# Performance work log

Measured on AMD Instinct MI355X. Metric: run time of the kernel, lower is better.

Reference implementation:

```python
import jax, jax.numpy as jnp
import numpy as np

B_, L_, O_, N_, S_, U_, DEL, HID, K = 16, 128, 128, 256, 64, 32, 64, 512, 4
D_OUT = DEL + N_ * U_ + N_ * S_  # 24640


def setup_inputs() -> dict:
    key = jax.random.key(0)
    ks = jax.random.split(key, 12)
    return {
        "x": jax.random.normal(ks[0], (B_, O_ + L_, S_), jnp.float32),
        "u": jax.random.normal(ks[1], (B_, 2 * L_, U_), jnp.float32),
        "A": jax.random.normal(ks[2], (N_, 1), jnp.float32) / 20.0,
        "W0": jax.random.normal(ks[3], (HID, S_), jnp.float32) * 0.05,
        "b0": jnp.zeros((HID,), jnp.float32),
        "W1": jax.random.normal(ks[4], (N_, HID), jnp.float32) * 0.05,
        "b1": jnp.zeros((N_,), jnp.float32),
        "conv_w": jax.random.normal(ks[5], (N_ + U_, 1, K), jnp.float32) * 0.3,
        "conv_b": jnp.zeros((N_ + U_,), jnp.float32),
        "Wg": jax.random.normal(ks[6], (D_OUT, N_ + U_), jnp.float32) * 0.05,
        "bg": jnp.zeros((D_OUT,), jnp.float32),
        "Wdt": jax.random.normal(ks[7], (N_, DEL), jnp.float32) * 0.05,
        "bdt": jnp.zeros((N_,), jnp.float32),
    }


def reference(x, u, A, W0, b0, W1, b1, conv_w, conv_b, Wg, bg, Wdt, bdt):
    def proj_x(v):  # Linear -> relu -> Linear (project_x)
        return jax.nn.relu(v @ W0.T + b0) @ W1.T + b1

    u = u[:, :, :U_]
    z0 = proj_x(x[:, O_ - 1, :])                       # (B, N)

    # ---- generate_matrices ----
    x_all = proj_x(x[:, :O_ - 1, :])                   # (B, O-1, N)
    u_all = u[:, :O_ - 1, :]                           # (B, O-1, U)
    old = jax.nn.silu(jnp.concatenate([x_all, u_all], axis=2))  # (B, O-1, N+U)
    old = jnp.transpose(old, (0, 2, 1))                # (B, N+U, O-1)
    old = jax.lax.conv_general_dilated(
        old, conv_w, window_strides=(1,), padding=[(K - 1, K - 1)],
        dimension_numbers=("NCH", "OIH", "NCH"), feature_group_count=N_ + U_,
    ) + conv_b[None, :, None]
    old = old[:, :, -L_:]                              # last L timesteps
    old = jax.nn.silu(jnp.transpose(old, (0, 2, 1)))   # (B, L, N+U)
    gen = old @ Wg.T + bg                              # (B, L, delta + N*U + N*S)
    delta, Bm, Cm = jnp.split(gen, [DEL, DEL + N_ * U_], axis=-1)
    delta = jax.nn.softplus(delta @ Wdt.T + bdt)       # (B, L, N)
    Bm = Bm.reshape(B_, L_, N_, U_)
    Cm = Cm.reshape(B_, L_, N_, S_)

    # ---- discretion_matrices ----
    a = A[:, 0]
    a = -jnp.where(a > 0, a, jnp.expm1(a))             # -celu(A), alpha=1
    dA = jnp.exp(delta * a)                            # (B, L, N)
    dB = ((dA - 1.0) * (1.0 / a))[..., None] * Bm      # (B, L, N, U)

    # ---- selective_scan ----
    u0 = u[:, O_ - 1:O_ - 1 + L_, :]                   # (B, L, U)
    xt = x[:, O_:O_ + L_, :]                           # (B, L, S) targets

    def step(z, inp):
        dAi, dBi, ui, Ci, xti = inp
        z = z * dAi + jnp.einsum("bnu,bu->bn", dBi, ui)
        y = jnp.einsum("bns,bn->bs", Ci, z)
        return z, (y, jnp.mean((y - xti) ** 2))

    xs = (
        jnp.swapaxes(dA, 0, 1), jnp.swapaxes(dB, 0, 1),
        jnp.swapaxes(u0, 0, 1), jnp.swapaxes(Cm, 0, 1), jnp.swapaxes(xt, 0, 1),
    )
    _, (ys, ls) = jax.lax.scan(step, z0, xs)
    loss = jnp.sum(ls) / L_
    return loss, jax.lax.stop_gradient(ys)             # ys: (L, B, S), detached as in torch
```

## Files before the change

### kernel.cpp

```cpp
#include <hip/hip_runtime.h>
#include <math.h>

#define B_   16
#define L_   128
#define O_   128
#define N_   256
#define S_   64
#define U_   32
#define DEL_ 64
#define HID_ 512
#define CH_  288
#define M_   2048
#define KD_  288
#define CM_BASE (DEL_ + N_*U_)
#define NSLICE 32

typedef __bf16 bf16_t;
typedef bf16_t bf16x8 __attribute__((ext_vector_type(8)));
typedef float  f32x4  __attribute__((ext_vector_type(4)));

#define AS1(p) ((const __attribute__((address_space(1))) void*)(unsigned long long)(const void*)(p))
#define AS3(p) ((__attribute__((address_space(3))) void*)(unsigned int)(unsigned long long)(const void*)(p))

__device__ __forceinline__ float silu_f(float x){ return x / (1.f + expf(-x)); }
__device__ __forceinline__ float softplus_f(float x){
  return fmaxf(x, 0.f) + log1pf(expf(-fabsf(x)));
}

__device__ __forceinline__ void cvt8(const float* src, bf16_t* dst){
  float4 a = ((const float4*)src)[0];
  float4 b = ((const float4*)src)[1];
  bf16x8 o;
  o[0]=(bf16_t)a.x; o[1]=(bf16_t)a.y; o[2]=(bf16_t)a.z; o[3]=(bf16_t)a.w;
  o[4]=(bf16_t)b.x; o[5]=(bf16_t)b.y; o[6]=(bf16_t)b.z; o[7]=(bf16_t)b.w;
  *(bf16x8*)dst = o;
}

#define CVT_BLOCKS 3465
#define W0_BLOCKS  16
#define W1_BLOCKS  64
#define XB_BLOCKS  64
__global__ void k_prep(const float* __restrict__ Wg, bf16_t* __restrict__ Wgbf,
                       const float* __restrict__ W0, bf16_t* __restrict__ W0bf,
                       const float* __restrict__ W1, bf16_t* __restrict__ W1bf,
                       const float* __restrict__ x,  bf16_t* __restrict__ xbf,
                       float* __restrict__ lossa){
  if (blockIdx.x == 0 && threadIdx.x < 2) lossa[threadIdx.x] = 0.f;
  if (blockIdx.x < CVT_BLOCKS) {
    int i = blockIdx.x*256 + threadIdx.x;
    if (i >= 887040) return;
    cvt8(Wg + (size_t)i*8, Wgbf + (size_t)i*8);
  } else if (blockIdx.x < CVT_BLOCKS + W0_BLOCKS) {
    int i = (blockIdx.x - CVT_BLOCKS)*256 + threadIdx.x;
    if (i >= 4096) return;
    cvt8(W0 + (size_t)i*8, W0bf + (size_t)i*8);
  } else if (blockIdx.x < CVT_BLOCKS + W0_BLOCKS + W1_BLOCKS) {
    int i = (blockIdx.x - CVT_BLOCKS - W0_BLOCKS)*256 + threadIdx.x;
    if (i >= 16384) return;
    cvt8(W1 + (size_t)i*8, W1bf + (size_t)i*8);
  } else {
    int i = (blockIdx.x - CVT_BLOCKS - W0_BLOCKS - W1_BLOCKS)*256 + threadIdx.x;
    if (i >= 16384) return;
    int m = i >> 3, c0 = (i & 7)*8;
    int b = m >> 7, t = m & 127;
    cvt8(x + (size_t)(((b<<8)+t)<<6) + c0, xbf + (size_t)m*64 + c0);
  }
}

#define STAGE64K(GBASE, ROW0G, STRIDE, KK, LDSP)                                     \
  { const bf16_t* gp_ = (GBASE) + (size_t)((ROW0G) + wave*16 + lm)*(STRIDE) + (KK) + lq*8; \
    __builtin_amdgcn_global_load_lds(AS1(gp_), AS3((LDSP) + wave*512), 16, 0, 0); }

#define STAGE128(GBASE, ROW0G, STRIDE, TT, BUF)                                      \
  { _Pragma("unroll")                                                                \
    for (int kb_ = 0; kb_ < 4; kb_++) {                                              \
      const bf16_t* gp_ = (GBASE) + (size_t)((ROW0G) + wave*16 + lm)*(STRIDE)        \
                          + (TT)*128 + kb_*32 + lq*8;                                \
      __builtin_amdgcn_global_load_lds(AS1(gp_), AS3((BUF) + kb_*2048 + wave*512), 16, 0, 0);\
    } }

#define STAGE32(GBASE, ROW0G, KK, LDSP)                                              \
  { _Pragma("unroll")                                                                \
    for (int l_ = 0; l_ < 2; l_++) {                                                 \
      int g_ = wave*2 + l_;                                                          \
      const bf16_t* gp_ = (GBASE) + (size_t)((ROW0G) + g_*16 + lm)*KD_ + (KK) + lq*8;\
      __builtin_amdgcn_global_load_lds(AS1(gp_), AS3((LDSP) + g_*512), 16, 0, 0);    \
    } }

#define STAGE_FR96(GBASE, ROW0G, KK, LDSP)                                           \
  { _Pragma("unroll")                                                                \
    for (int c_ = 0; c_ < 3; c_++) {                                                 \
      _Pragma("unroll")                                                              \
      for (int q_ = 0; q_ < 2; q_++) {                                               \
        int g_ = wave*2 + q_;                                                        \
        const bf16_t* gp_ = (GBASE) + (size_t)((ROW0G) + g_*16 + lm)*KD_ + (KK) + c_*32 + lq*8;\
        __builtin_amdgcn_global_load_lds(AS1(gp_), AS3((LDSP) + c_*4096 + g_*512), 16, 0, 0);\
      } } }

__global__ __launch_bounds__(256) void k_mlp1m(
    const bf16_t* __restrict__ xbf, const bf16_t* __restrict__ W0bf,
    const float* __restrict__ b0, bf16_t* __restrict__ Hbf){
  __shared__ __align__(16) bf16_t As[2][2048];
  __shared__ __align__(16) bf16_t Bs[2][2048];
  int tid = threadIdx.x;
  int wave = tid >> 6, lane = tid & 63;
  int wm = wave & 1, wn = wave >> 1;
  int nt = blockIdx.x, mt = blockIdx.y;
  int m0 = mt*64, n0 = nt*64;
  int lm = lane & 15, lq = lane >> 4;

  f32x4 acc[2][2];
  #pragma unroll
  for (int i=0;i<2;i++)
    #pragma unroll
    for (int j=0;j<2;j++){ acc[i][j][0]=0.f;acc[i][j][1]=0.f;acc[i][j][2]=0.f;acc[i][j][3]=0.f; }

  STAGE64K(xbf,  m0, 64, 0, As[0]);
  STAGE64K(W0bf, n0, 64, 0, Bs[0]);
  __syncthreads();
  #pragma unroll
  for (int t = 0; t < 2; ++t) {
    int cur = t & 1;
    if (t < 1) {
      STAGE64K(xbf,  m0, 64, 32, As[1]);
      STAGE64K(W0bf, n0, 64, 32, Bs[1]);
    }
    bf16x8 af[2], bff[2];
    #pragma unroll
    for (int i=0;i<2;i++) af[i]  = *(const bf16x8*)&As[cur][(wm*2 + i)*512 + lane*8];
    #pragma unroll
    for (int j=0;j<2;j++) bff[j] = *(const bf16x8*)&Bs[cur][(wn*2 + j)*512 + lane*8];
    #pragma unroll
    for (int i=0;i<2;i++)
      #pragma unroll
      for (int j=0;j<2;j++)
        acc[i][j] = __builtin_amdgcn_mfma_f32_16x16x32_bf16(af[i], bff[j], acc[i][j], 0,0,0);
    __syncthreads();
  }
  #pragma unroll
  for (int i=0;i<2;i++)
    #pragma unroll
    for (int j=0;j<2;j++){
      int col = n0 + wn*32 + j*16 + lm;
      float bb = b0[col];
      #pragma unroll
      for (int r=0;r<4;r++){
        int row = m0 + wm*32 + i*16 + lq*4 + r;
        Hbf[(size_t)row*HID_ + col] = (bf16_t)fmaxf(acc[i][j][r] + bb, 0.f);
      }
    }
}

__global__ __launch_bounds__(256) void k_mlp2m(
    const bf16_t* __restrict__ Hbf, const bf16_t* __restrict__ W1bf,
    const float* __restrict__ b1, float* __restrict__ P){
  __shared__ __align__(16) bf16_t As[2][8192];
  __shared__ __align__(16) bf16_t Bs[2][8192];
  int tid = threadIdx.x;
  int wave = tid >> 6, lane = tid & 63;
  int wm = wave & 1, wn = wave >> 1;
  int nt = blockIdx.x, mt = blockIdx.y;
  int m0 = mt*64, n0 = nt*64;
  int lm = lane & 15, lq = lane >> 4;

  f32x4 acc[2][2];
  #pragma unroll
  for (int i=0;i<2;i++)
    #pragma unroll
    for (int j=0;j<2;j++){ acc[i][j][0]=0.f;acc[i][j][1]=0.f;acc[i][j][2]=0.f;acc[i][j][3]=0.f; }

  STAGE128(Hbf,  m0, HID_, 0, As[0]);
  STAGE128(W1bf, n0, HID_, 0, Bs[0]);
  __syncthreads();
  #pragma unroll
  for (int t = 0; t < 4; ++t) {
    int cur = t & 1;
    if (t < 3) {
      STAGE128(Hbf,  m0, HID_, t+1, As[cur^1]);
      STAGE128(W1bf, n0, HID_, t+1, Bs[cur^1]);
    }
    #pragma unroll
    for (int kb = 0; kb < 4; kb++) {
      bf16x8 af[2], bff[2];
      #pragma unroll
      for (int i=0;i<2;i++) af[i]  = *(const bf16x8*)&As[cur][kb*2048 + (wm*2 + i)*512 + lane*8];
      #pragma unroll
      for (int j=0;j<2;j++) bff[j] = *(const bf16x8*)&Bs[cur][kb*2048 + (wn*2 + j)*512 + lane*8];
      #pragma unroll
      for (int i=0;i<2;i++)
        #pragma unroll
        for (int j=0;j<2;j++)
          acc[i][j] = __builtin_amdgcn_mfma_f32_16x16x32_bf16(af[i], bff[j], acc[i][j], 0,0,0);
    }
    __syncthreads();
  }
  #pragma unroll
  for (int i=0;i<2;i++)
    #pragma unroll
    for (int j=0;j<2;j++){
      int col = n0 + wn*32 + j*16 + lm;
      float bb = b1[col];
      #pragma unroll
      for (int r=0;r<4;r++){
        int row = m0 + wm*32 + i*16 + lq*4 + r;
        P[(size_t)row*N_ + col] = acc[i][j][r] + bb;
      }
    }
}

__global__ __launch_bounds__(256) void k_convdelta(
    const float* __restrict__ P, const float* __restrict__ u,
    const float* __restrict__ cw, const float* __restrict__ cb,
    const float* __restrict__ Wg, const float* __restrict__ bg,
    const float* __restrict__ Wdt, const float* __restrict__ bdt,
    const float* __restrict__ Ap, bf16_t* __restrict__ oldbf,
    float* __restrict__ dA, float* __restrict__ coef){
  __shared__ __align__(16) float olds[4*KD_];
  __shared__ float dr[4][64];
  int tid = threadIdx.x;
  int m0 = blockIdx.x * 4;
  int b = m0 >> 7, l0 = m0 & 127;
  for (int e = tid; e < 4*CH_; e += 256) {
    int r = e / CH_, c = e - r*CH_;
    int l = l0 + r;
    float acc = cb[c];
    #pragma unroll
    for (int k = 0; k < 4; k++) {
      int t = l + k - 1;
      if (t >= 0 && t <= O_-2) {
        float s = (c < N_) ? P[((b<<7)+t)*N_ + c] : u[((b<<8)+t)*U_ + (c-N_)];
        acc += silu_f(s) * cw[c*4 + k];
      }
    }
    float v = silu_f(acc);
    olds[e] = v;
    oldbf[(size_t)(m0+r)*CH_ + c] = (bf16_t)v;
  }
  __syncthreads();
  {
    int d = tid & 63;
    int r = tid >> 6;
    const float* wrow = Wg + (size_t)d*KD_;
    const float* orow = olds + r*KD_;
    float s = 0.f;
    for (int k = 0; k < KD_; k++) s += orow[k] * wrow[k];
    dr[r][d] = s + bg[d];
  }
  __syncthreads();
  int n = tid;
  float wrow[64];
  #pragma unroll
  for (int d = 0; d < 64; d++) wrow[d] = Wdt[n*64 + d];
  float a0 = Ap[n];
  float a = -(a0 > 0.f ? a0 : expm1f(a0));
  float inva = 1.f / a;
  float bd = bdt[n];
  #pragma unroll
  for (int r = 0; r < 4; r++) {
    float s = bd;
    #pragma unroll
    for (int d = 0; d < 64; d++) s += dr[r][d] * wrow[d];
    float dd = softplus_f(s);
    float e  = expf(dd * a);
    size_t m = m0 + r;
    dA[m*N_ + n]   = e;
    coef[m*N_ + n] = (e - 1.f) * inva;
  }
}

__global__ __launch_bounds__(256, 2) void k_bmfma(
    const bf16_t* __restrict__ oldbf, const bf16_t* __restrict__ Wgbf,
    const float* __restrict__ bg, const float* __restrict__ u,
    const float* __restrict__ coef, const float* __restrict__ dAg,
    const float* __restrict__ Pg, float* __restrict__ zall){
  __shared__ union {
    struct { __align__(16) bf16_t A[2][4096]; __align__(16) bf16_t B[2][4096]; } st;
    struct { float wl[128][4]; float dal[128][4]; } sc;
  } sm;
  int tid = threadIdx.x;
  int wave = tid >> 6, lane = tid & 63;
  int wm = wave & 1, wn = wave >> 1;
  int mt = blockIdx.y, nt = blockIdx.x;
  int m0 = mt*128, ncol0 = nt*128;
  int lm = lane & 15, lq = lane >> 4;

  f32x4 acc[4][4];
  #pragma unroll
  for (int i=0;i<4;i++)
    #pragma unroll
    for (int j=0;j<4;j++){ acc[i][j][0]=0.f;acc[i][j][1]=0.f;acc[i][j][2]=0.f;acc[i][j][3]=0.f; }

  STAGE32(oldbf, m0, 0, sm.st.A[0]);
  STAGE32(Wgbf, DEL_ + ncol0, 0, sm.st.B[0]);
  __syncthreads();
  for (int t = 0; t < 9; ++t) {
    int cur = t & 1;
    if (t < 8) {
      int kk = (t+1)*32;
      STAGE32(oldbf, m0, kk, sm.st.A[cur^1]);
      STAGE32(Wgbf, DEL_ + ncol0, kk, sm.st.B[cur^1]);
    }
    bf16x8 af[4], bff[4];
    #pragma unroll
    for (int i=0;i<4;i++) af[i]  = *(const bf16x8*)&sm.st.A[cur][(wm*4 + i)*512 + lane*8];
    #pragma unroll
    for (int j=0;j<4;j++) bff[j] = *(const bf16x8*)&sm.st.B[cur][(wn*4 + j)*512 + lane*8];
    __builtin_amdgcn_s_setprio(1);
    #pragma unroll
    for (int i=0;i<4;i++)
      #pragma unroll
      for (int j=0;j<4;j++)
        acc[i][j] = __builtin_amdgcn_mfma_f32_16x16x32_bf16(af[i], bff[j], acc[i][j], 0,0,0);
    __builtin_amdgcn_s_setprio(0);
    __syncthreads();
  }

  for (int e = tid; e < 512; e += 256)
    sm.sc.dal[e>>2][e&3] = dAg[(size_t)(m0 + (e>>2))*N_ + nt*4 + (e&3)];

  float bgv[4];
  #pragma unroll
  for (int j=0;j<4;j++) bgv[j] = bg[DEL_ + ncol0 + wn*64 + j*16 + lm];
  float p[2][4][4];
  #pragma unroll
  for (int a=0;a<2;a++)
    #pragma unroll
    for (int i=0;i<4;i++)
      #pragma unroll
      for (int r=0;r<4;r++) p[a][i][r]=0.f;
  #pragma unroll
  for (int i=0;i<4;i++){
    #pragma unroll
    for (int r=0;r<4;r++){
      int m = m0 + wm*64 + i*16 + lq*4 + r;
      int b = m >> 7, l = m & 127;
      const float* urow = u + ((size_t)(b<<8) + 127 + l)*U_;
      #pragma unroll
      for (int j=0;j<4;j++){
        float uu = urow[(j&1)*16 + lm];
        p[j>>1][i][r] += (acc[i][j][r] + bgv[j]) * uu;
      }
    }
  }
  #pragma unroll
  for (int mk = 1; mk < 16; mk <<= 1){
    #pragma unroll
    for (int a=0;a<2;a++)
      #pragma unroll
      for (int i=0;i<4;i++)
        #pragma unroll
        for (int r=0;r<4;r++) p[a][i][r] += __shfl_xor(p[a][i][r], mk);
  }
  if (lm == 0){
    #pragma unroll
    for (int nl=0;nl<2;nl++){
      int n = ((ncol0 + wn*64 + nl*32) >> 5);
      int nc = wn*2 + nl;
      #pragma unroll
      for (int i=0;i<4;i++)
        #pragma unroll
        for (int r=0;r<4;r++){
          int l = wm*64 + i*16 + lq*4 + r;
          sm.sc.wl[l][nc] = coef[(size_t)(m0+l)*N_ + n] * p[nl][i][r];
        }
    }
  }
  __syncthreads();

  {
    int nc = wave;
    int n = nt*4 + nc;
    float z0 = Pg[(size_t)(m0 + 127)*N_ + n];
    int l0 = lane*2;
    float a0 = sm.sc.dal[l0][nc],   w0 = sm.sc.wl[l0][nc];
    float a1 = sm.sc.dal[l0+1][nc], w1 = sm.sc.wl[l0+1][nc];
    float A = a0*a1, Bv = w0*a1 + w1;
    #pragma unroll
    for (int d = 1; d < 64; d <<= 1){
      float Ap = __shfl_up(A, d);
      float Bp = __shfl_up(Bv, d);
      if (lane >= d){ Bv = Bp*A + Bv; A = Ap*A; }
    }
    float Ae = __shfl_up(A, 1);
    float Be = __shfl_up(Bv, 1);
    if (lane == 0){ Ae = 1.f; Be = 0.f; }
    float zp = z0*Ae + Be;
    float za = zp*a0 + w0;
    float zb = za*a1 + w1;
    zall[(size_t)(m0 + l0)*N_ + n]     = za;
    zall[(size_t)(m0 + l0 + 1)*N_ + n] = zb;
  }
}

__global__ __launch_bounds__(256, 2) void k_cmfma(
    const bf16_t* __restrict__ oldbf, const bf16_t* __restrict__ Wgbf,
    const float* __restrict__ bg, const float* __restrict__ zall,
    float* __restrict__ ypart){
  __shared__ union {
    struct { __align__(16) bf16_t A[3*4096];
             __align__(16) bf16_t Bb[3*4096];
             float zl[128][8]; } st;
    float ylds[128][64];
  } sm;
  int tid = threadIdx.x;
  int wave = tid >> 6, lane = tid & 63;
  int wm = wave & 1, wn = wave >> 1;
  int mt = blockIdx.y, grp = blockIdx.x;
  int m0 = mt*128;
  int lm = lane & 15, lq = lane >> 4;

  for (int e = tid; e < 1024; e += 256)
    sm.st.zl[e>>3][e&7] = zall[(size_t)(m0 + (e>>3))*N_ + grp*8 + (e&7)];

  f32x4 yacc[4][4];
  #pragma unroll
  for (int i=0;i<4;i++)
    #pragma unroll
    for (int j=0;j<4;j++){ yacc[i][j][0]=0.f;yacc[i][j][1]=0.f;yacc[i][j][2]=0.f;yacc[i][j][3]=0.f; }

  for (int kh = 0; kh < 3; kh++) {
    int kk = kh*96;
    STAGE_FR96(oldbf, m0, kk, sm.st.A);
    for (int it = 0; it < 4; it++) {
      int ncol0 = (grp*4 + it)*128;
      STAGE_FR96(Wgbf, CM_BASE + ncol0, kk, sm.st.Bb);
      __syncthreads();
      f32x4 acc[4][4];
      #pragma unroll
      for (int i=0;i<4;i++)
        #pragma unroll
        for (int j=0;j<4;j++){ acc[i][j][0]=0.f;acc[i][j][1]=0.f;acc[i][j][2]=0.f;acc[i][j][3]=0.f; }
      __builtin_amdgcn_s_setprio(1);
      for (int c = 0; c < 3; c++) {
        bf16x8 af[4], bff[4];
        #pragma unroll
        for (int i=0;i<4;i++) af[i]  = *(const bf16x8*)&sm.st.A[c*4096 + (wm*4 + i)*512 + lane*8];
        #pragma unroll
        for (int j=0;j<4;j++) bff[j] = *(const bf16x8*)&sm.st.Bb[c*4096 + (wn*4 + j)*512 + lane*8];
        #pragma unroll
        for (int i=0;i<4;i++)
          #pragma unroll
          for (int j=0;j<4;j++)
            acc[i][j] = __builtin_amdgcn_mfma_f32_16x16x32_bf16(af[i], bff[j], acc[i][j], 0,0,0);
      }
      __builtin_amdgcn_s_setprio(0);
      int nl = it*2 + wn;
      float bgv[4];
      #pragma unroll
      for (int j=0;j<4;j++)
        bgv[j] = (kh == 2) ? bg[CM_BASE + ncol0 + wn*64 + j*16 + lm] : 0.f;
      #pragma unroll
      for (int i=0;i<4;i++){
        #pragma unroll
        for (int r=0;r<4;r++){
          float zv = sm.st.zl[wm*64 + i*16 + lq*4 + r][nl];
          #pragma unroll
          for (int j=0;j<4;j++)
            yacc[i][j][r] += (acc[i][j][r] + bgv[j]) * zv;
        }
      }
      __syncthreads();
    }
  }

  if (wn == 1){
    #pragma unroll
    for (int i=0;i<4;i++)
      #pragma unroll
      for (int j=0;j<4;j++)
        #pragma unroll
        for (int r=0;r<4;r++){
          int ml = wm*64 + i*16 + lq*4 + r;
          sm.ylds[ml][j*16 + lm] = yacc[i][j][r];
        }
  }
  __syncthreads();
  if (wn == 0){
    float* dst = ypart + (size_t)grp*(M_*S_);
    #pragma unroll
    for (int i=0;i<4;i++)
      #pragma unroll
      for (int j=0;j<4;j++)
        #pragma unroll
        for (int r=0;r<4;r++){
          int ml = wm*64 + i*16 + lq*4 + r;
          int s = j*16 + lm;
          dst[(size_t)(m0+ml)*S_ + s] = yacc[i][j][r] + sm.ylds[ml][s];
        }
  }
}

__global__ void k_finalize(const float* __restrict__ ypart, const float* __restrict__ x,
                           float* __restrict__ out, float* __restrict__ lossacc){
  __shared__ float red[256];
  int tid = threadIdx.x;
  float ls = 0.f;
  #pragma unroll
  for (int q = 0; q < 2; q++) {
    int e = blockIdx.x*512 + q*256 + tid;
    int m = e >> 6, s = e & 63;
    int b = m >> 7, l = m & 127;
    float yv = 0.f;
    #pragma unroll 8
    for (int g = 0; g < NSLICE; g++) yv += ypart[(size_t)g*(M_*S_) + e];
    out[1 + (size_t)((l<<4) + b)*S_ + s] = yv;
    float xv = x[((size_t)(b<<8) + 128 + l)*S_ + s];
    float d = yv - xv;
    ls += d*d;
  }
  red[tid] = ls; __syncthreads();
  for (int st = 128; st > 0; st >>= 1) {
    if (tid < st) red[tid] += red[tid+st];
    __syncthreads();
  }
  if (tid == 0) {
    atomicAdd(&lossacc[0], red[0]);
    __threadfence();
    unsigned old = atomicAdd((unsigned*)&lossacc[1], 1u);
    if (old == 255u) {
      float tot = atomicAdd(&lossacc[0], 0.f);
      out[0] = tot * (1.f / (float)(B_*S_*L_));
    }
  }
}

extern "C" void kernel_launch(void* const* d_in, const int* in_sizes, int n_in,
                              void* d_out, int out_size, void* d_ws, size_t ws_size,
                              hipStream_t stream) {
  const float* x   = (const float*)d_in[0];
  const float* u   = (const float*)d_in[1];
  const float* Ap  = (const float*)d_in[2];
  const float* W0  = (const float*)d_in[3];
  const float* b0  = (const float*)d_in[4];
  const float* W1  = (const float*)d_in[5];
  const float* b1  = (const float*)d_in[6];
  const float* cw  = (const float*)d_in[7];
  const float* cb  = (const float*)d_in[8];
  const float* Wg  = (const float*)d_in[9];
  const float* bg  = (const float*)d_in[10];
  const float* Wdt = (const float*)d_in[11];
  const float* bdt = (const float*)d_in[12];
  float* out = (float*)d_out;

  float* ws    = (float*)d_ws;
  float* zall  = ws;
  float* lossa = zall + 524288;
  bf16_t* oldbf = (bf16_t*)(lossa + 512);
  bf16_t* Wgbf  = (bf16_t*)(lossa + 512 + 294912);
  bf16_t* W0bf  = (bf16_t*)(lossa + 512 + 294912 + 3548160);
  bf16_t* W1bf  = (bf16_t*)(lossa + 512 + 294912 + 3548160 + 16384);
  bf16_t* xbf   = (bf16_t*)(lossa + 512 + 294912 + 3548160 + 16384 + 65536);
  bf16_t* Hbf   = (bf16_t*)(lossa + 512 + 294912 + 3548160 + 16384 + 65536 + 65536);
  float* R     = lossa + 512 + 294912 + 3548160 + 16384 + 65536 + 65536 + 524288;
  float* Pp    = R;
  float* dA    = Pp   + 524288;
  float* coef  = dA   + 524288;
  float* ypart = R;

  k_prep<<<CVT_BLOCKS + W0_BLOCKS + W1_BLOCKS + XB_BLOCKS, 256, 0, stream>>>(
      Wg, Wgbf, W0, W0bf, W1, W1bf, x, xbf, lossa);
  k_mlp1m<<<dim3(HID_/64, M_/64), 256, 0, stream>>>(xbf, W0bf, b0, Hbf);
  k_mlp2m<<<dim3(N_/64, M_/64), 256, 0, stream>>>(Hbf, W1bf, b1, Pp);
  k_convdelta<<<M_/4, 256, 0, stream>>>(Pp, u, cw, cb, Wg, bg, Wdt, bdt, Ap,
                                        oldbf, dA, coef);
  k_bmfma<<<dim3(64, 16), 256, 0, stream>>>(oldbf, Wgbf, bg, u, coef, dA, Pp, zall);
  k_cmfma<<<dim3(32, 16), 256, 0, stream>>>(oldbf, Wgbf, bg, zall, ypart);
  k_finalize<<<256, 256, 0, stream>>>(ypart, x, out, lossa);
}
```

Before: 201.7 us.

## Pipeline Wg tile staging with a 4-deep LDS ring in C-matrix MFMA kernel

Replaces the per-iteration synchronous staging of the Wg B-tile (stage 96 K-columns, then sync, then compute) with a 4-slot ring of 32-column chunks. Loads run two chunks ahead and use explicit vmcnt waits and raw barriers, so global-to-LDS traffic overlaps the MFMA work. This removes the exposed load latency and the double __syncthreads per tile. In exchange it adds LDS usage and relies on hand-tuned vmcnt counts, which assume a fixed number of outstanding loads per STAGE32.

```diff
diff --git a/kernel.cpp b/kernel.cpp
--- a/kernel.cpp
+++ b/kernel.cpp
@@ -398,7 +398,7 @@
     float* __restrict__ ypart){
   __shared__ union {
     struct { __align__(16) bf16_t A[3*4096];
-             __align__(16) bf16_t Bb[3*4096];
+             __align__(16) bf16_t Bb[4][4096];
              float zl[128][8]; } st;
     float ylds[128][64];
   } sm;
@@ -418,51 +418,67 @@
     #pragma unroll
     for (int j=0;j<4;j++){ yacc[i][j][0]=0.f;yacc[i][j][1]=0.f;yacc[i][j][2]=0.f;yacc[i][j][3]=0.f; }
 
+  f32x4 acc[4][4];
   for (int kh = 0; kh < 3; kh++) {
     int kk = kh*96;
+    if (kh) __builtin_amdgcn_s_barrier();
     STAGE_FR96(oldbf, m0, kk, sm.st.A);
-    for (int it = 0; it < 4; it++) {
-      int ncol0 = (grp*4 + it)*128;
-      STAGE_FR96(Wgbf, CM_BASE + ncol0, kk, sm.st.Bb);
-      __syncthreads();
-      f32x4 acc[4][4];
-      #pragma unroll
-      for (int i=0;i<4;i++)
-        #pragma unroll
-        for (int j=0;j<4;j++){ acc[i][j][0]=0.f;acc[i][j][1]=0.f;acc[i][j][2]=0.f;acc[i][j][3]=0.f; }
-      __builtin_amdgcn_s_setprio(1);
-      for (int c = 0; c < 3; c++) {
-        bf16x8 af[4], bff[4];
-        #pragma unroll
-        for (int i=0;i<4;i++) af[i]  = *(const bf16x8*)&sm.st.A[c*4096 + (wm*4 + i)*512 + lane*8];
-        #pragma unroll
-        for (int j=0;j<4;j++) bff[j] = *(const bf16x8*)&sm.st.Bb[c*4096 + (wn*4 + j)*512 + lane*8];
+    STAGE32(Wgbf, CM_BASE + (grp*4)*128, kk,      sm.st.Bb[0]);
+    STAGE32(Wgbf, CM_BASE + (grp*4)*128, kk + 32, sm.st.Bb[1]);
+    asm volatile("s_waitcnt vmcnt(0)" ::: "memory");
+    __builtin_amdgcn_s_barrier();
+
+    #pragma unroll
+    for (int c = 0; c < 12; ++c) {
+      int it = c/3, cb = c%3;
+      if (c + 2 < 12) {
+        int c2 = c + 2, it2 = c2/3, cb2 = c2%3;
+        STAGE32(Wgbf, CM_BASE + (grp*4 + it2)*128, kk + cb2*32, sm.st.Bb[c2 & 3]);
+      }
+      if (c <= 9)       { asm volatile("s_waitcnt vmcnt(4)" ::: "memory"); }
+      else if (c == 10) { asm volatile("s_waitcnt vmcnt(2)" ::: "memory"); }
+      else              { asm volatile("s_waitcnt vmcnt(0)" ::: "memory"); }
+      __builtin_amdgcn_s_barrier();
+      if (cb == 0) {
         #pragma unroll
         for (int i=0;i<4;i++)
           #pragma unroll
-          for (int j=0;j<4;j++)
-            acc[i][j] = __builtin_amdgcn_mfma_f32_16x16x32_bf16(af[i], bff[j], acc[i][j], 0,0,0);
-      }
+          for (int j=0;j<4;j++){ acc[i][j][0]=0.f;acc[i][j][1]=0.f;acc[i][j][2]=0.f;acc[i][j][3]=0.f; }
+      }
+      bf16x8 af[4], bff[4];
+      #pragma unroll
+      for (int i=0;i<4;i++) af[i]  = *(const bf16x8*)&sm.st.A[cb*4096 + (wm*4 + i)*512 + lane*8];
+      #pragma unroll
+      for (int j=0;j<4;j++) bff[j] = *(const bf16x8*)&sm.st.Bb[c & 3][(wn*4 + j)*512 + lane*8];
+      __builtin_amdgcn_s_setprio(1);
+      #pragma unroll
+      for (int i=0;i<4;i++)
+        #pragma unroll
+        for (int j=0;j<4;j++)
+          acc[i][j] = __builtin_amdgcn_mfma_f32_16x16x32_bf16(af[i], bff[j], acc[i][j], 0,0,0);
       __builtin_amdgcn_s_setprio(0);
-      int nl = it*2 + wn;
-      float bgv[4];
-      #pragma unroll
-      for (int j=0;j<4;j++)
-        bgv[j] = (kh == 2) ? bg[CM_BASE + ncol0 + wn*64 + j*16 + lm] : 0.f;
-      #pragma unroll
-      for (int i=0;i<4;i++){
-        #pragma unroll
-        for (int r=0;r<4;r++){
-          float zv = sm.st.zl[wm*64 + i*16 + lq*4 + r][nl];
+      if (cb == 2) {
+        int ncol0 = (grp*4 + it)*128;
+        int nl = it*2 + wn;
+        float bgv[4];
+        #pragma unroll
+        for (int j=0;j<4;j++)
+          bgv[j] = (kh == 2) ? bg[CM_BASE + ncol0 + wn*64 + j*16 + lm] : 0.f;
+        #pragma unroll
+        for (int i=0;i<4;i++){
           #pragma unroll
-          for (int j=0;j<4;j++)
-            yacc[i][j][r] += (acc[i][j][r] + bgv[j]) * zv;
+          for (int r=0;r<4;r++){
+            float zv = sm.st.zl[wm*64 + i*16 + lq*4 + r][nl];
+            #pragma unroll
+            for (int j=0;j<4;j++)
+              yacc[i][j][r] += (acc[i][j][r] + bgv[j]) * zv;
+          }
         }
       }
-      __syncthreads();
-    }
-  }
-
+    }
+  }
+
+  __builtin_amdgcn_s_barrier();
   if (wn == 1){
     #pragma unroll
     for (int i=0;i<4;i++)
```

After: 203.2 us. About the same (+0.8%).
